# Kernel optimization log

Measured on AMD Instinct MI355X. Metric: run time of the kernel, lower is better.

Reference implementation:

```python
import jax, jax.numpy as jnp
import numpy as np

H = 128   # hidden_dim
L = 3     # num_layers
N = 50000
E = 800000
EPS = 1e-5


def setup_inputs() -> dict:
    key = jax.random.key(0)
    ks = jax.random.split(key, 16)
    s = 0.02  # param init scale
    return {
        "edge_index_new": jax.random.randint(ks[0], (2, E), 0, N),
        "aligned_features": jax.random.normal(ks[1], (E, 8), jnp.float32),
        "h_nodes_old": jax.random.normal(ks[2], (N, H), jnp.float32),
        "num_nodes": N,
        # node_fusion: Linear(2H -> H)
        "Wf": jax.random.normal(ks[3], (2 * H, H), jnp.float32) * s,
        "bf": jnp.zeros((H,), jnp.float32),
        # edge_to_weight: Linear(8->H), Linear(H->1)
        "We1": jax.random.normal(ks[4], (8, H), jnp.float32) * s,
        "be1": jnp.zeros((H,), jnp.float32),
        "We2": jax.random.normal(ks[5], (H, 1), jnp.float32) * s,
        "be2": jnp.zeros((1,), jnp.float32),
        # GraphConv per layer: lin_rel (W+b), lin_root (W, no bias)
        "Wrel": jax.random.normal(ks[6], (L, H, H), jnp.float32) * s,
        "brel": jnp.zeros((L, H), jnp.float32),
        "Wroot": jax.random.normal(ks[7], (L, H, H), jnp.float32) * s,
        # LayerNorm per layer
        "gamma": jnp.ones((L, H), jnp.float32),
        "beta": jnp.zeros((L, H), jnp.float32),
        # edge_decoder: Linear(2H+8 -> H), Linear(H -> 1)
        "Wd1": jax.random.normal(ks[8], (2 * H + 8, H), jnp.float32) * s,
        "bd1": jnp.zeros((H,), jnp.float32),
        "Wd2": jax.random.normal(ks[9], (H, 1), jnp.float32) * s,
        "bd2": jnp.zeros((1,), jnp.float32),
    }


def _layer_norm(x, g, b):
    mu = jnp.mean(x, axis=-1, keepdims=True)
    var = jnp.mean((x - mu) ** 2, axis=-1, keepdims=True)
    return (x - mu) * jax.lax.rsqrt(var + EPS) * g + b


def reference(edge_index_new, aligned_features, h_nodes_old, num_nodes,
              Wf, bf, We1, be1, We2, be2,
              Wrel, brel, Wroot, gamma, beta,
              Wd1, bd1, Wd2, bd2):
    dt = h_nodes_old.dtype
    hd = Wf.shape[1]
    # node_fusion(cat([ones, h_old])) ; dropout is identity in eval
    x_init = jnp.ones((num_nodes, hd), dtype=dt)
    x = jax.nn.relu(jnp.concatenate([x_init, h_nodes_old], axis=-1) @ Wf + bf)
    # edge_to_weight -> scalar per edge
    ew = jax.nn.sigmoid(jax.nn.relu(aligned_features @ We1 + be1) @ We2 + be2)[:, 0]
    src, dst = edge_index_new[0], edge_index_new[1]
    n_layers = Wrel.shape[0]
    for l in range(n_layers):
        x_res = x
        # GraphConv: sum_{j->i} w_e * x[j], then lin_rel(agg) + lin_root(x)
        msg = ew[:, None] * x[src]                         # [E, H]
        agg = jax.ops.segment_sum(msg, dst, num_segments=num_nodes)
        h = agg @ Wrel[l] + brel[l] + x @ Wroot[l]
        h = jax.nn.relu(_layer_norm(h, gamma[l], beta[l]))
        x = h + x_res
    # edge decoder on gathered node pairs + raw 8-dim features
    edge_repr = jnp.concatenate([x[src], x[dst], aligned_features], axis=-1)
    hmid = jax.nn.relu(edge_repr @ Wd1 + bd1)
    return hmid @ Wd2 + bd2
```

## Files before the change

### kernel.cpp

```cpp
#include <hip/hip_runtime.h>
#include <hip/hip_bf16.h>

#define H 128
#define LN_EPS 1e-5f

typedef __attribute__((ext_vector_type(8))) short bf16x8;
typedef __attribute__((ext_vector_type(4))) float f32x4;

static __device__ __forceinline__ unsigned short f2bf(float f) {
  unsigned u = __float_as_uint(f);
  unsigned r = (u + 0x7fff + ((u >> 16) & 1)) >> 16;
  return (unsigned short)r;
}
static __device__ __forceinline__ float bf2f(unsigned short s) {
  return __uint_as_float(((unsigned)s) << 16);
}


__global__ void zero_int_kernel(int* __restrict__ p, int n) {
  int i = blockIdx.x * blockDim.x + threadIdx.x;
  if (i < n) p[i] = 0;
}

__global__ __launch_bounds__(1024) void prep_cvec_kernel(const float* __restrict__ Wf,
                                                         const float* __restrict__ bf,
                                                         float* __restrict__ cvec) {
  __shared__ float part[8][128];
  int tid = threadIdx.x;
  int col = tid & 127, seg = tid >> 7;
  float s = 0.f;
  for (int r = seg * 16; r < seg * 16 + 16; ++r) s += Wf[r * H + col];
  part[seg][col] = s;
  __syncthreads();
  if (tid < 128) {
    float t = bf[tid];
#pragma unroll
    for (int g = 0; g < 8; ++g) t += part[g][tid];
    cvec[tid] = t;
  }
}

__global__ void count_kernel(const int* __restrict__ ei, int E, int* __restrict__ cnt) {
  int e = blockIdx.x * blockDim.x + threadIdx.x;
  if (e < E) atomicAdd(&cnt[ei[E + e]], 1);
}

__global__ __launch_bounds__(1024) void scan_kernel(const int* __restrict__ cnt,
                                                    int* __restrict__ off,
                                                    int* __restrict__ pos, int N) {
  __shared__ int wtot[16];
  __shared__ int wbase[16];
  __shared__ int s_btot;
  __shared__ int s_carry;
  int tid = threadIdx.x, lane = tid & 63, wid = tid >> 6;
  if (tid == 0) s_carry = 0;
  __syncthreads();
  for (int base = 0; base < N; base += 4096) {
    int i0 = base + tid * 4;
    int v[4];
#pragma unroll
    for (int j = 0; j < 4; ++j) v[j] = (i0 + j < N) ? cnt[i0 + j] : 0;
    int s = v[0] + v[1] + v[2] + v[3];
    int incl = s;
#pragma unroll
    for (int o = 1; o < 64; o <<= 1) {
      int t = __shfl_up(incl, o, 64);
      if (lane >= o) incl += t;
    }
    if (lane == 63) wtot[wid] = incl;
    __syncthreads();
    if (tid == 0) {
      int run = 0;
      for (int w = 0; w < 16; ++w) { wbase[w] = run; run += wtot[w]; }
      s_btot = run;
    }
    __syncthreads();
    int e0 = s_carry + wbase[wid] + (incl - s);
#pragma unroll
    for (int j = 0; j < 4; ++j) {
      if (i0 + j < N) { off[i0 + j] = e0; pos[i0 + j] = e0; }
      e0 += v[j];
    }
    __syncthreads();
    if (tid == 0) s_carry += s_btot;
    __syncthreads();
  }
  if (tid == 0) off[N] = s_carry;
}

__global__ __launch_bounds__(256) void pack_w_kernel(const float* __restrict__ Wf,
                                                     const float* __restrict__ Wrel,
                                                     const float* __restrict__ Wroot,
                                                     const float* __restrict__ Wd1,
                                                     unsigned short* __restrict__ wpk) {
  int id = blockIdx.x * blockDim.x + threadIdx.x;
  if (id >= 9 * 2048) return;
  int l = id & 63, nf = (id >> 6) & 7, kk = (id >> 9) & 3, m = id >> 11;
  const float* src;
  if (m == 0) src = Wf + H * H;
  else if (m <= 3) src = Wrel + (size_t)(m - 1) * H * H;
  else if (m <= 6) src = Wroot + (size_t)(m - 4) * H * H;
  else src = Wd1 + (size_t)(m - 7) * H * H;
  int col = nf * 16 + (l & 15);
  int kbase = kk * 32 + (l >> 4) * 8;
  unsigned short t[8];
#pragma unroll
  for (int j = 0; j < 8; ++j) t[j] = f2bf(src[(size_t)(kbase + j) * H + col]);
  *(uint4*)&wpk[(size_t)id * 8] = *(uint4*)t;
}

__global__ __launch_bounds__(256) void edge_weight_v3_kernel(
    const float* __restrict__ af, const float* __restrict__ We1, const float* __restrict__ be1,
    const float* __restrict__ We2, const float* __restrict__ be2, float* __restrict__ ew, int E) {
  int lane = threadIdx.x & 63;
  int sub = lane & 15;
  int grp = lane >> 4;
  float w1[8][8], b1[8], w2[8];
#pragma unroll
  for (int i = 0; i < 8; ++i)
#pragma unroll
    for (int c = 0; c < 8; ++c) w1[i][c] = We1[i * H + sub * 8 + c];
#pragma unroll
  for (int c = 0; c < 8; ++c) { b1[c] = be1[sub * 8 + c]; w2[c] = We2[sub * 8 + c]; }
  float b2 = be2[0];
  int gw = (blockIdx.x * blockDim.x + threadIdx.x) >> 6;
  int nw = (gridDim.x * blockDim.x) >> 6;
  int n4 = (E + 3) >> 2;
  for (int e4 = gw; e4 < n4; e4 += nw) {
    int e = e4 * 4 + grp;
    bool valid = e < E;
    int ee = valid ? e : E - 1;
    float4 a0 = *(const float4*)&af[(size_t)ee * 8];
    float4 a1 = *(const float4*)&af[(size_t)ee * 8 + 4];
    float afv[8] = {a0.x, a0.y, a0.z, a0.w, a1.x, a1.y, a1.z, a1.w};
    float t[8];
#pragma unroll
    for (int c = 0; c < 8; ++c) t[c] = b1[c];
#pragma unroll
    for (int i = 0; i < 8; ++i)
#pragma unroll
      for (int c = 0; c < 8; ++c) t[c] += afv[i] * w1[i][c];
    float p = 0.f;
#pragma unroll
    for (int c = 0; c < 8; ++c) p += fmaxf(t[c], 0.f) * w2[c];
    p += __shfl_xor(p, 1, 64);
    p += __shfl_xor(p, 2, 64);
    p += __shfl_xor(p, 4, 64);
    p += __shfl_xor(p, 8, 64);
    if (valid && sub == 0) {
      float s = p + b2;
      ew[e] = 1.f / (1.f + expf(-s));
    }
  }
}

__global__ void fill_v2_kernel(const int* __restrict__ ei, const float* __restrict__ ew, int E,
                               int* __restrict__ pos, uint4* __restrict__ csr4) {
  int e = blockIdx.x * blockDim.x + threadIdx.x;
  if (e < E) {
    int d = ei[E + e];
    int p = atomicAdd(&pos[d], 1);
    csr4[p] = make_uint4((unsigned)ei[e], __float_as_uint(ew[e]), (unsigned)e, (unsigned)d);
  }
}

__global__ __launch_bounds__(256) void gemm_init_kernel(
    const float* __restrict__ Xf, const unsigned short* __restrict__ Wp,
    const float* __restrict__ bias, unsigned short* __restrict__ Y, int M) {
  int l = threadIdx.x & 63, w = threadIdx.x >> 6;
  int lr = l & 15, lg = l >> 4;
  int m0 = blockIdx.x * 128 + w * 32;
  f32x4 acc[2][8] = {};
  for (int kk = 0; kk < 4; ++kk) {
    bf16x8 a[2];
#pragma unroll
    for (int mi = 0; mi < 2; ++mi) {
      int row = m0 + mi * 16 + lr;
      if (row >= M) row = M - 1;
      const float* xp = &Xf[(size_t)row * H + kk * 32 + lg * 8];
      float4 u0 = *(const float4*)xp;
      float4 u1 = *(const float4*)(xp + 4);
      unsigned short t[8] = {f2bf(u0.x), f2bf(u0.y), f2bf(u0.z), f2bf(u0.w),
                             f2bf(u1.x), f2bf(u1.y), f2bf(u1.z), f2bf(u1.w)};
      a[mi] = *(const bf16x8*)t;
    }
#pragma unroll
    for (int nf = 0; nf < 8; ++nf) {
      bf16x8 b = *(const bf16x8*)&Wp[(size_t)(kk * 8 + nf) * 512 + l * 8];
#pragma unroll
      for (int mi = 0; mi < 2; ++mi)
        acc[mi][nf] = __builtin_amdgcn_mfma_f32_16x16x32_bf16(a[mi], b, acc[mi][nf], 0, 0, 0);
    }
  }
  float bv[8];
#pragma unroll
  for (int nf = 0; nf < 8; ++nf) bv[nf] = bias[nf * 16 + lr];
#pragma unroll
  for (int mi = 0; mi < 2; ++mi)
#pragma unroll
    for (int r = 0; r < 4; ++r) {
      int row = m0 + mi * 16 + lg * 4 + r;
      if (row < M) {
#pragma unroll
        for (int nf = 0; nf < 8; ++nf)
          Y[(size_t)row * H + nf * 16 + lr] = f2bf(fmaxf(acc[mi][nf][r] + bv[nf], 0.f));
      }
    }
}

__global__ __launch_bounds__(256) void gemm_layer_ln_kernel(
    const unsigned short* __restrict__ Agg, const unsigned short* __restrict__ WpRel,
    unsigned short* __restrict__ Xio, const unsigned short* __restrict__ WpRoot,
    const float* __restrict__ brel, const float* __restrict__ gamma,
    const float* __restrict__ beta, int M) {
  int l = threadIdx.x & 63, w = threadIdx.x >> 6;
  int lr = l & 15, lg = l >> 4;
  int m0 = blockIdx.x * 128 + w * 32;
  f32x4 acc[2][8] = {};
  for (int kk = 0; kk < 8; ++kk) {
    const unsigned short* X = (kk >= 4) ? Xio : Agg;
    const unsigned short* Wp = (kk >= 4) ? WpRoot : WpRel;
    int k4 = kk & 3;
    bf16x8 a[2] = {};
#pragma unroll
    for (int mi = 0; mi < 2; ++mi) {
      int row = m0 + mi * 16 + lr;
      if (row < M) a[mi] = *(const bf16x8*)&X[(size_t)row * H + k4 * 32 + lg * 8];
    }
#pragma unroll
    for (int nf = 0; nf < 8; ++nf) {
      bf16x8 b = *(const bf16x8*)&Wp[(size_t)(k4 * 8 + nf) * 512 + l * 8];
#pragma unroll
      for (int mi = 0; mi < 2; ++mi)
        acc[mi][nf] = __builtin_amdgcn_mfma_f32_16x16x32_bf16(a[mi], b, acc[mi][nf], 0, 0, 0);
    }
  }
  float bv[8], gv[8], bev[8];
#pragma unroll
  for (int nf = 0; nf < 8; ++nf) {
    int col = nf * 16 + lr;
    bv[nf] = brel[col]; gv[nf] = gamma[col]; bev[nf] = beta[col];
  }
#pragma unroll
  for (int mi = 0; mi < 2; ++mi) {
#pragma unroll
    for (int r = 0; r < 4; ++r) {
      int row = m0 + mi * 16 + lg * 4 + r;
      float hv[8], s1 = 0.f;
#pragma unroll
      for (int nf = 0; nf < 8; ++nf) { hv[nf] = acc[mi][nf][r] + bv[nf]; s1 += hv[nf]; }
      s1 += __shfl_xor(s1, 1, 64);
      s1 += __shfl_xor(s1, 2, 64);
      s1 += __shfl_xor(s1, 4, 64);
      s1 += __shfl_xor(s1, 8, 64);
      float mu = s1 * (1.0f / H);
      float s2 = 0.f;
#pragma unroll
      for (int nf = 0; nf < 8; ++nf) { float d = hv[nf] - mu; s2 += d * d; }
      s2 += __shfl_xor(s2, 1, 64);
      s2 += __shfl_xor(s2, 2, 64);
      s2 += __shfl_xor(s2, 4, 64);
      s2 += __shfl_xor(s2, 8, 64);
      float rstd = rsqrtf(s2 * (1.0f / H) + LN_EPS);
      if (row < M) {
#pragma unroll
        for (int nf = 0; nf < 8; ++nf) {
          int col = nf * 16 + lr;
          float v = fmaxf((hv[nf] - mu) * rstd * gv[nf] + bev[nf], 0.f);
          v += bf2f(Xio[(size_t)row * H + col]);
          Xio[(size_t)row * H + col] = f2bf(v);
        }
      }
    }
  }
}

__global__ __launch_bounds__(256) void gemm_dec_kernel(
    const unsigned short* __restrict__ X, const unsigned short* __restrict__ WpA,
    const unsigned short* __restrict__ WpB, const float* __restrict__ bd1,
    unsigned short* __restrict__ Aout, unsigned short* __restrict__ Bout, int M) {
  int l = threadIdx.x & 63, w = threadIdx.x >> 6;
  int lr = l & 15, lg = l >> 4;
  int m0 = blockIdx.x * 128 + w * 32;
  f32x4 accA[2][8] = {};
  f32x4 accB[2][8] = {};
  for (int kk = 0; kk < 4; ++kk) {
    bf16x8 a[2];
#pragma unroll
    for (int mi = 0; mi < 2; ++mi) {
      int row = m0 + mi * 16 + lr;
      if (row >= M) row = M - 1;
      a[mi] = *(const bf16x8*)&X[(size_t)row * H + kk * 32 + lg * 8];
    }
#pragma unroll
    for (int nf = 0; nf < 8; ++nf) {
      bf16x8 bA = *(const bf16x8*)&WpA[(size_t)(kk * 8 + nf) * 512 + l * 8];
      bf16x8 bB = *(const bf16x8*)&WpB[(size_t)(kk * 8 + nf) * 512 + l * 8];
#pragma unroll
      for (int mi = 0; mi < 2; ++mi) {
        accA[mi][nf] = __builtin_amdgcn_mfma_f32_16x16x32_bf16(a[mi], bA, accA[mi][nf], 0, 0, 0);
        accB[mi][nf] = __builtin_amdgcn_mfma_f32_16x16x32_bf16(a[mi], bB, accB[mi][nf], 0, 0, 0);
      }
    }
  }
  float bdv[8];
#pragma unroll
  for (int nf = 0; nf < 8; ++nf) bdv[nf] = bd1[nf * 16 + lr];
#pragma unroll
  for (int mi = 0; mi < 2; ++mi)
#pragma unroll
    for (int r = 0; r < 4; ++r) {
      int row = m0 + mi * 16 + lg * 4 + r;
      if (row < M) {
#pragma unroll
        for (int nf = 0; nf < 8; ++nf) {
          int col = nf * 16 + lr;
          Aout[(size_t)row * H + col] = f2bf(accA[mi][nf][r] + bdv[nf]);
          Bout[(size_t)row * H + col] = f2bf(accB[mi][nf][r]);
        }
      }
    }
}

__global__ __launch_bounds__(256) void gather_agg_v3_kernel(
    const unsigned short* __restrict__ xbf, const int* __restrict__ off,
    const uint4* __restrict__ csr4, unsigned short* __restrict__ aggbf, int N) {
  int gw = (blockIdx.x * blockDim.x + threadIdx.x) >> 6;
  int lane = threadIdx.x & 63;
  int half = lane >> 5, li = lane & 31;
  int n = gw * 2 + half;
  if (n < N) {
    int s0 = off[n], s1 = off[n + 1];
    float a0 = 0.f, a1 = 0.f, a2 = 0.f, a3 = 0.f;
    for (int base = s0; base < s1; base += 16) {
      uint2 c[16];
#pragma unroll
      for (int j = 0; j < 16; ++j) {
        int id = base + j;
        c[j] = *(const uint2*)&csr4[id < s1 ? id : s1 - 1];
        if (id >= s1) c[j].y = 0;
      }
      uint2 v[16];
#pragma unroll
      for (int j = 0; j < 16; ++j)
        v[j] = *(const uint2*)&xbf[(size_t)c[j].x * H + li * 4];
#pragma unroll
      for (int j = 0; j < 16; ++j) {
        float w = __uint_as_float(c[j].y);
        a0 += w * bf2f((unsigned short)(v[j].x & 0xffffu));
        a1 += w * bf2f((unsigned short)(v[j].x >> 16));
        a2 += w * bf2f((unsigned short)(v[j].y & 0xffffu));
        a3 += w * bf2f((unsigned short)(v[j].y >> 16));
      }
    }
    unsigned o0 = (unsigned)f2bf(a0) | ((unsigned)f2bf(a1) << 16);
    unsigned o1 = (unsigned)f2bf(a2) | ((unsigned)f2bf(a3) << 16);
    *(uint2*)&aggbf[(size_t)n * H + li * 4] = make_uint2(o0, o1);
  }
}

__global__ __launch_bounds__(256) void edge_out_v6_kernel(
    const uint4* __restrict__ csr4, const float* __restrict__ af,
    const unsigned short* __restrict__ A, const unsigned short* __restrict__ B,
    const float* __restrict__ Wd1c, const float* __restrict__ Wd2,
    const float* __restrict__ bd2, float* __restrict__ out, int E) {
  int lane = threadIdx.x & 63;
  int sub = lane & 15;
  int grp = lane >> 4;
  float wc[8][8], w2[8];
#pragma unroll
  for (int i = 0; i < 8; ++i)
#pragma unroll
    for (int c = 0; c < 8; ++c) wc[i][c] = Wd1c[i * H + sub * 8 + c];
#pragma unroll
  for (int c = 0; c < 8; ++c) w2[c] = Wd2[sub * 8 + c];
  float b2 = bd2[0];
  int gw = (blockIdx.x * blockDim.x + threadIdx.x) >> 6;
  int nw = (gridDim.x * blockDim.x) >> 6;
  int n4 = (E + 3) >> 2;
  for (int e4 = gw; e4 < n4; e4 += nw) {
    int idx = e4 * 4 + grp;
    bool valid = idx < E;
    int ii = valid ? idx : E - 1;
    uint4 c = csr4[ii];
    uint4 va = *(const uint4*)&A[(size_t)c.x * H + sub * 8];
    uint4 vb = *(const uint4*)&B[(size_t)c.w * H + sub * 8];
    float4 f0 = *(const float4*)&af[(size_t)c.z * 8];
    float4 f1 = *(const float4*)&af[(size_t)c.z * 8 + 4];
    const unsigned* pa = (const unsigned*)&va;
    const unsigned* pb = (const unsigned*)&vb;
    float t[8];
#pragma unroll
    for (int q = 0; q < 4; ++q) {
      t[q * 2 + 0] = bf2f((unsigned short)(pa[q] & 0xffffu)) + bf2f((unsigned short)(pb[q] & 0xffffu));
      t[q * 2 + 1] = bf2f((unsigned short)(pa[q] >> 16)) + bf2f((unsigned short)(pb[q] >> 16));
    }
    float afv[8] = {f0.x, f0.y, f0.z, f0.w, f1.x, f1.y, f1.z, f1.w};
#pragma unroll
    for (int i = 0; i < 8; ++i)
#pragma unroll
      for (int cc = 0; cc < 8; ++cc) t[cc] += afv[i] * wc[i][cc];
    float p = 0.f;
#pragma unroll
    for (int cc = 0; cc < 8; ++cc) p += fmaxf(t[cc], 0.f) * w2[cc];
    p += __shfl_xor(p, 1, 64);
    p += __shfl_xor(p, 2, 64);
    p += __shfl_xor(p, 4, 64);
    p += __shfl_xor(p, 8, 64);
    if (valid && sub == 0) out[c.z] = p + b2;
  }
}

extern "C" void kernel_launch(void* const* d_in, const int* in_sizes, int n_in, void* d_out,
                              int out_size, void* d_ws, size_t ws_size, hipStream_t stream) {
  const int* ei = (const int*)d_in[0];
  const float* af = (const float*)d_in[1];
  const float* h_old = (const float*)d_in[2];
  const float* Wf = (const float*)d_in[4];
  const float* bf = (const float*)d_in[5];
  const float* We1 = (const float*)d_in[6];
  const float* be1 = (const float*)d_in[7];
  const float* We2 = (const float*)d_in[8];
  const float* be2 = (const float*)d_in[9];
  const float* Wrel = (const float*)d_in[10];
  const float* brel = (const float*)d_in[11];
  const float* Wroot = (const float*)d_in[12];
  const float* gamma = (const float*)d_in[13];
  const float* beta = (const float*)d_in[14];
  const float* Wd1 = (const float*)d_in[15];
  const float* bd1 = (const float*)d_in[16];
  const float* Wd2 = (const float*)d_in[17];
  const float* bd2 = (const float*)d_in[18];
  const int N = in_sizes[2] / H;
  const int E = in_sizes[1] / 8;
  float* out = (float*)d_out;

  char* p = (char*)d_ws;
  auto alloc = [&](size_t b) { char* r = p; p += (b + 255) & ~(size_t)255; return r; };
  int* cnt = (int*)alloc((size_t)N * 4);
  int* pos = (int*)alloc((size_t)N * 4);
  int* off = (int*)alloc((size_t)(N + 1) * 4);
  uint4* csr4 = (uint4*)alloc((size_t)E * 16);
  float* ew = (float*)alloc((size_t)E * 4);
  float* cvec = (float*)alloc(H * 4);
  unsigned short* wpk = (unsigned short*)alloc((size_t)9 * 16384 * 2);
  unsigned short* xbf = (unsigned short*)alloc((size_t)N * H * 2);
  unsigned short* aggbf = (unsigned short*)alloc((size_t)N * H * 2);
  unsigned short* buf2 = (unsigned short*)alloc((size_t)N * H * 2);

  unsigned short* Abf = aggbf;
  unsigned short* Bbf = buf2;

  hipLaunchKernelGGL(zero_int_kernel, dim3((N + 255) / 256), dim3(256), 0, stream, cnt, N);
  hipLaunchKernelGGL(prep_cvec_kernel, dim3(1), dim3(1024), 0, stream, Wf, bf, cvec);
  hipLaunchKernelGGL(count_kernel, dim3((E + 255) / 256), dim3(256), 0, stream, ei, E, cnt);
  hipLaunchKernelGGL(scan_kernel, dim3(1), dim3(1024), 0, stream, cnt, off, pos, N);
  hipLaunchKernelGGL(edge_weight_v3_kernel, dim3(4096), dim3(256), 0, stream, af, We1, be1,
                     We2, be2, ew, E);
  hipLaunchKernelGGL(fill_v2_kernel, dim3((E + 255) / 256), dim3(256), 0, stream, ei, ew, E,
                     pos, csr4);
  hipLaunchKernelGGL(pack_w_kernel, dim3(72), dim3(256), 0, stream, Wf, Wrel, Wroot, Wd1, wpk);

  int gblocks = (N + 127) / 128;
  hipLaunchKernelGGL(gemm_init_kernel, dim3(gblocks), dim3(256), 0, stream, h_old, wpk, cvec,
                     xbf, N);

  int gat_blocks = (N / 2 + 3) / 4;
  for (int l = 0; l < 3; ++l) {
    hipLaunchKernelGGL(gather_agg_v3_kernel, dim3(gat_blocks), dim3(256), 0, stream, xbf, off,
                       csr4, aggbf, N);
    hipLaunchKernelGGL(gemm_layer_ln_kernel, dim3(gblocks), dim3(256), 0, stream, aggbf,
                       wpk + (size_t)(1 + l) * 16384, xbf, wpk + (size_t)(4 + l) * 16384,
                       brel + l * H, gamma + l * H, beta + l * H, N);
  }

  hipLaunchKernelGGL(gemm_dec_kernel, dim3(gblocks), dim3(256), 0, stream, xbf,
                     wpk + (size_t)7 * 16384, wpk + (size_t)8 * 16384, bd1, Abf, Bbf, N);
  hipLaunchKernelGGL(edge_out_v6_kernel, dim3(4096), dim3(256), 0, stream, csr4, af, Abf, Bbf,
                     Wd1 + 2 * H * H, Wd2, bd2, out, E);
}
```

Baseline: 478.8 us.

## Fuse neighbor aggregation gather into per-layer GEMM+LayerNorm kernel via LDS

Each layer now runs one kernel. Every wave gathers weighted neighbor sums for its 32 rows into shared memory, then feeds them straight into the MFMA GEMM and LayerNorm epilogue. This removes the aggbf global write/read round-trip and one launch per layer. Ping-pong x buffers replace in-place updates so other blocks can still gather from the previous layer's features. The cost is less parallelism in the gather phase, since one wave processes 32 rows serially with 2 rows per iteration, and the added LDS use may lower occupancy for the latency-bound gather.

```diff
diff --git a/kernel.cpp b/kernel.cpp
--- a/kernel.cpp
+++ b/kernel.cpp
@@ -208,25 +208,63 @@
     }
 }
 
-__global__ __launch_bounds__(256) void gemm_layer_ln_kernel(
-    const unsigned short* __restrict__ Agg, const unsigned short* __restrict__ WpRel,
-    unsigned short* __restrict__ Xio, const unsigned short* __restrict__ WpRoot,
+__global__ __launch_bounds__(256) void layer_fused_kernel(
+    const unsigned short* __restrict__ Xin, unsigned short* __restrict__ Xout,
+    const int* __restrict__ off, const uint4* __restrict__ csr4,
+    const unsigned short* __restrict__ WpRel, const unsigned short* __restrict__ WpRoot,
     const float* __restrict__ brel, const float* __restrict__ gamma,
     const float* __restrict__ beta, int M) {
+  __shared__ unsigned short sAgg[4][32][136];
   int l = threadIdx.x & 63, w = threadIdx.x >> 6;
+  int m0 = blockIdx.x * 128 + w * 32;
+  int half = l >> 5, li = l & 31;
+  for (int it = 0; it < 16; ++it) {
+    int rl = it * 2 + half;
+    int n = m0 + rl;
+    if (n < M) {
+      int s0 = off[n], s1 = off[n + 1];
+      float a0 = 0.f, a1 = 0.f, a2 = 0.f, a3 = 0.f;
+      for (int base = s0; base < s1; base += 16) {
+        uint2 c[16];
+#pragma unroll
+        for (int j = 0; j < 16; ++j) {
+          int id = base + j;
+          c[j] = *(const uint2*)&csr4[id < s1 ? id : s1 - 1];
+          if (id >= s1) c[j].y = 0;
+        }
+        uint2 v[16];
+#pragma unroll
+        for (int j = 0; j < 16; ++j)
+          v[j] = *(const uint2*)&Xin[(size_t)c[j].x * H + li * 4];
+#pragma unroll
+        for (int j = 0; j < 16; ++j) {
+          float wgt = __uint_as_float(c[j].y);
+          a0 += wgt * bf2f((unsigned short)(v[j].x & 0xffffu));
+          a1 += wgt * bf2f((unsigned short)(v[j].x >> 16));
+          a2 += wgt * bf2f((unsigned short)(v[j].y & 0xffffu));
+          a3 += wgt * bf2f((unsigned short)(v[j].y >> 16));
+        }
+      }
+      unsigned o0 = (unsigned)f2bf(a0) | ((unsigned)f2bf(a1) << 16);
+      unsigned o1 = (unsigned)f2bf(a2) | ((unsigned)f2bf(a3) << 16);
+      *(uint2*)&sAgg[w][rl][li * 4] = make_uint2(o0, o1);
+    }
+  }
   int lr = l & 15, lg = l >> 4;
-  int m0 = blockIdx.x * 128 + w * 32;
   f32x4 acc[2][8] = {};
   for (int kk = 0; kk < 8; ++kk) {
-    const unsigned short* X = (kk >= 4) ? Xio : Agg;
-    const unsigned short* Wp = (kk >= 4) ? WpRoot : WpRel;
+    bool rel = kk < 4;
     int k4 = kk & 3;
     bf16x8 a[2] = {};
 #pragma unroll
     for (int mi = 0; mi < 2; ++mi) {
       int row = m0 + mi * 16 + lr;
-      if (row < M) a[mi] = *(const bf16x8*)&X[(size_t)row * H + k4 * 32 + lg * 8];
-    }
+      if (row < M) {
+        if (rel) a[mi] = *(const bf16x8*)&sAgg[w][mi * 16 + lr][k4 * 32 + lg * 8];
+        else     a[mi] = *(const bf16x8*)&Xin[(size_t)row * H + k4 * 32 + lg * 8];
+      }
+    }
+    const unsigned short* Wp = rel ? WpRel : WpRoot;
 #pragma unroll
     for (int nf = 0; nf < 8; ++nf) {
       bf16x8 b = *(const bf16x8*)&Wp[(size_t)(k4 * 8 + nf) * 512 + l * 8];
@@ -267,8 +305,8 @@
         for (int nf = 0; nf < 8; ++nf) {
           int col = nf * 16 + lr;
           float v = fmaxf((hv[nf] - mu) * rstd * gv[nf] + bev[nf], 0.f);
-          v += bf2f(Xio[(size_t)row * H + col]);
-          Xio[(size_t)row * H + col] = f2bf(v);
+          v += bf2f(Xin[(size_t)row * H + col]);
+          Xout[(size_t)row * H + col] = f2bf(v);
         }
       }
     }
@@ -320,43 +358,6 @@
         }
       }
     }
-}
-
-__global__ __launch_bounds__(256) void gather_agg_v3_kernel(
-    const unsigned short* __restrict__ xbf, const int* __restrict__ off,
-    const uint4* __restrict__ csr4, unsigned short* __restrict__ aggbf, int N) {
-  int gw = (blockIdx.x * blockDim.x + threadIdx.x) >> 6;
-  int lane = threadIdx.x & 63;
-  int half = lane >> 5, li = lane & 31;
-  int n = gw * 2 + half;
-  if (n < N) {
-    int s0 = off[n], s1 = off[n + 1];
-    float a0 = 0.f, a1 = 0.f, a2 = 0.f, a3 = 0.f;
-    for (int base = s0; base < s1; base += 16) {
-      uint2 c[16];
-#pragma unroll
-      for (int j = 0; j < 16; ++j) {
-        int id = base + j;
-        c[j] = *(const uint2*)&csr4[id < s1 ? id : s1 - 1];
-        if (id >= s1) c[j].y = 0;
-      }
-      uint2 v[16];
-#pragma unroll
-      for (int j = 0; j < 16; ++j)
-        v[j] = *(const uint2*)&xbf[(size_t)c[j].x * H + li * 4];
-#pragma unroll
-      for (int j = 0; j < 16; ++j) {
-        float w = __uint_as_float(c[j].y);
-        a0 += w * bf2f((unsigned short)(v[j].x & 0xffffu));
-        a1 += w * bf2f((unsigned short)(v[j].x >> 16));
-        a2 += w * bf2f((unsigned short)(v[j].y & 0xffffu));
-        a3 += w * bf2f((unsigned short)(v[j].y >> 16));
-      }
-    }
-    unsigned o0 = (unsigned)f2bf(a0) | ((unsigned)f2bf(a1) << 16);
-    unsigned o1 = (unsigned)f2bf(a2) | ((unsigned)f2bf(a3) << 16);
-    *(uint2*)&aggbf[(size_t)n * H + li * 4] = make_uint2(o0, o1);
-  }
 }
 
 __global__ __launch_bounds__(256) void edge_out_v6_kernel(
@@ -444,12 +445,9 @@
   float* ew = (float*)alloc((size_t)E * 4);
   float* cvec = (float*)alloc(H * 4);
   unsigned short* wpk = (unsigned short*)alloc((size_t)9 * 16384 * 2);
-  unsigned short* xbf = (unsigned short*)alloc((size_t)N * H * 2);
-  unsigned short* aggbf = (unsigned short*)alloc((size_t)N * H * 2);
+  unsigned short* xA = (unsigned short*)alloc((size_t)N * H * 2);
+  unsigned short* xB = (unsigned short*)alloc((size_t)N * H * 2);
   unsigned short* buf2 = (unsigned short*)alloc((size_t)N * H * 2);
-
-  unsigned short* Abf = aggbf;
-  unsigned short* Bbf = buf2;
 
   hipLaunchKernelGGL(zero_int_kernel, dim3((N + 255) / 256), dim3(256), 0, stream, cnt, N);
   hipLaunchKernelGGL(prep_cvec_kernel, dim3(1), dim3(1024), 0, stream, Wf, bf, cvec);
@@ -463,18 +461,20 @@
 
   int gblocks = (N + 127) / 128;
   hipLaunchKernelGGL(gemm_init_kernel, dim3(gblocks), dim3(256), 0, stream, h_old, wpk, cvec,
-                     xbf, N);
-
-  int gat_blocks = (N / 2 + 3) / 4;
+                     xA, N);
+
+  unsigned short* xin = xA;
+  unsigned short* xout = xB;
   for (int l = 0; l < 3; ++l) {
-    hipLaunchKernelGGL(gather_agg_v3_kernel, dim3(gat_blocks), dim3(256), 0, stream, xbf, off,
-                       csr4, aggbf, N);
-    hipLaunchKernelGGL(gemm_layer_ln_kernel, dim3(gblocks), dim3(256), 0, stream, aggbf,
-                       wpk + (size_t)(1 + l) * 16384, xbf, wpk + (size_t)(4 + l) * 16384,
+    hipLaunchKernelGGL(layer_fused_kernel, dim3(gblocks), dim3(256), 0, stream, xin, xout, off,
+                       csr4, wpk + (size_t)(1 + l) * 16384, wpk + (size_t)(4 + l) * 16384,
                        brel + l * H, gamma + l * H, beta + l * H, N);
-  }
-
-  hipLaunchKernelGGL(gemm_dec_kernel, dim3(gblocks), dim3(256), 0, stream, xbf,
+    unsigned short* tmp = xin; xin = xout; xout = tmp;
+  }
+  unsigned short* Abf = xout;
+  unsigned short* Bbf = buf2;
+
+  hipLaunchKernelGGL(gemm_dec_kernel, dim3(gblocks), dim3(256), 0, stream, xin,
                      wpk + (size_t)7 * 16384, wpk + (size_t)8 * 16384, bd1, Abf, Bbf, N);
   hipLaunchKernelGGL(edge_out_v6_kernel, dim3(4096), dim3(256), 0, stream, csr4, af, Abf, Bbf,
                      Wd1 + 2 * H * H, Wd2, bd2, out, E);
```

Result: slower. 508.3 us (+6.2%).
